# Kernel tuning notes

Measured on AMD Instinct MI355X. Metric: run time of the kernel, lower is better.

The kernel has to match this reference:

```python
import jax, jax.numpy as jnp
import numpy as np

N = 100000      # nodes
E = 1600000     # edges (avg degree 16)
EMB = 128
L = 3           # num_layers
NUM_OPS = 64
MAX_BW = 64     # max_bitwidth
P = 4           # max_num_params


def setup_inputs() -> dict:
    key = jax.random.key(0)
    ks = jax.random.split(key, 24)
    w = lambda k, s: jax.random.normal(k, s, jnp.float32) * 0.05
    return {
        "ops": jax.random.randint(ks[0], (N,), 0, NUM_OPS),
        "params": jax.random.randint(ks[1], (N, P), 0, MAX_BW),
        "edge_src": jax.random.randint(ks[2], (E,), 0, N),
        "edge_dst": jax.random.randint(ks[3], (E,), 0, N),
        "op_emb_table": w(ks[4], (NUM_OPS, EMB)),
        "param_emb_table": w(ks[5], (MAX_BW, EMB)),
        "opmlp_w1": w(ks[6], ((1 + P) * EMB, EMB)), "opmlp_b1": w(ks[7], (EMB,)),
        "opmlp_w2": w(ks[8], (EMB, EMB)), "opmlp_b2": w(ks[9], (EMB,)),
        "conv_w": w(ks[10], (L, EMB, EMB)), "conv_b": w(ks[11], (L, EMB)),
        "mlp_w1": w(ks[12], (L * EMB, EMB)), "mlp_b1": w(ks[13], (EMB,)),
        "mlp_w2": w(ks[14], (EMB, EMB)), "mlp_b2": w(ks[15], (EMB,)),
        "mlpinv_w1": w(ks[16], (L * EMB, EMB)), "mlpinv_b1": w(ks[17], (EMB,)),
        "mlpinv_w2": w(ks[18], (EMB, EMB)), "mlpinv_b2": w(ks[19], (EMB,)),
        "comb_w": w(ks[20], (2 * EMB, EMB)), "comb_b": w(ks[21], (EMB,)),
    }


def _lrelu(x):
    return jax.nn.leaky_relu(x)  # slope 0.01, matches nn.LeakyReLU default


def _gin_mean(feat, src, dst, w, b):
    # DGL GINConv(aggregator='mean', eps=0): apply_func(feat + mean_in_neighbors(feat))
    n = feat.shape[0]
    msg = jax.ops.segment_sum(feat[src], dst, num_segments=n)           # [N, EMB]
    deg = jax.ops.segment_sum(jnp.ones(src.shape, feat.dtype), dst, num_segments=n)
    agg = msg / jnp.maximum(deg, 1.0)[:, None]
    return _lrelu((feat + agg) @ w + b)


def reference(ops, params, edge_src, edge_dst,
              op_emb_table, param_emb_table,
              opmlp_w1, opmlp_b1, opmlp_w2, opmlp_b2,
              conv_w, conv_b,
              mlp_w1, mlp_b1, mlp_w2, mlp_b2,
              mlpinv_w1, mlpinv_b1, mlpinv_w2, mlpinv_b2,
              comb_w, comb_b):
    n = ops.shape[0]
    # OpEmb: cat([op_emb] + per-param embs) -> MLP
    op_e = op_emb_table[ops]                               # [N, EMB]
    par_e = param_emb_table[params].reshape(n, -1)         # [N, P*EMB]
    h = jnp.concatenate([op_e, par_e], axis=1)
    h = _lrelu(h @ opmlp_w1 + opmlp_b1) @ opmlp_w2 + opmlp_b2
    states = h
    states_inv = h  # op_emb called twice on same inputs in the original

    conv_outs = []
    for i in range(L):
        states = _gin_mean(states, edge_src, edge_dst, conv_w[i], conv_b[i])
        conv_outs.append(states.sum(axis=0))
    final_sum = states.sum(axis=0)

    conv_outs_inv = []
    for i in range(L):
        states_inv = _gin_mean(states_inv, edge_dst, edge_src, conv_w[i], conv_b[i])
        # NOTE: original code appends states.sum(dim=0) (the final forward states),
        # not states_inv -- faithfully reproduced.
        conv_outs_inv.append(final_sum)

    g_emb = _lrelu(jnp.concatenate(conv_outs) @ mlp_w1 + mlp_b1) @ mlp_w2 + mlp_b2
    g_inv_emb = _lrelu(jnp.concatenate(conv_outs_inv) @ mlpinv_w1 + mlpinv_b1) @ mlpinv_w2 + mlpinv_b2

    out1 = jnp.concatenate([g_emb, g_inv_emb]) @ comb_w + comb_b          # [EMB]
    out2 = jnp.concatenate([states, states_inv], axis=1) @ comb_w + comb_b  # [N, EMB]
    return (out1, out2)
```

## Files before the change

### kernel.cpp

```cpp
#include <hip/hip_runtime.h>


typedef unsigned int  uint;
typedef unsigned short ushort;
typedef float  f32x4  __attribute__((ext_vector_type(4)));
typedef short  bf16x8 __attribute__((ext_vector_type(8)));

#define ABITS 9
#define CAPB  12288
#define CHUNK 2048

__device__ __forceinline__ float lrelu(float x) { return x > 0.0f ? x : 0.01f * x; }
__device__ __forceinline__ ushort f2b(float x) {
    uint u = __float_as_uint(x);
    return (ushort)((u + 0x7fffu + ((u >> 16) & 1u)) >> 16);
}
__device__ __forceinline__ float lof(uint u) { return __uint_as_float(u << 16); }
__device__ __forceinline__ float hif(uint u) { return __uint_as_float(u & 0xffff0000u); }

__global__ void tables_kernel(const float* __restrict__ opT, const float* __restrict__ parT,
                              const float* __restrict__ W1, float* __restrict__ A)
{
    int b = blockIdx.x;
    int t = b >> 6, v = b & 63, j = threadIdx.x;
    const float* emb = (t == 0 ? opT : parT) + v * 128;
    const float* w = W1 + (size_t)t * 128 * 128;
    float acc = 0.f;
    for (int k = 0; k < 128; ++k) acc += emb[k] * w[k * 128 + j];
    A[(size_t)b * 128 + j] = acc;
}

__global__ void prep_w(const float* __restrict__ convw, const float* __restrict__ ow2,
                       const float* __restrict__ cw, ushort* __restrict__ Wt)
{
    int t = blockIdx.x * 256 + threadIdx.x;
    int img = t >> 14, idx = t & 16383;
    int k = idx >> 7, c = idx & 127;
    const float* src;
    if (img < 3)      src = convw + img * 16384;
    else if (img == 3) src = ow2;
    else              src = cw + (img - 4) * 16384;
    float v = src[k * 128 + c];
    int byteoff = (img << 15) + (c << 8) + ((((k >> 3) ^ (c & 7)) << 4)) + ((k & 7) << 1);
    Wt[byteoff >> 1] = f2b(v);
}

__global__ __launch_bounds__(256) void binpass_kernel(
    const int* __restrict__ esrc, const int* __restrict__ edst, int E, int nb,
    int* __restrict__ gcur, uint2* __restrict__ binbuf)
{
    __shared__ int hist[448];
    __shared__ int lstart[448];
    __shared__ int gbase[448];
    __shared__ int lcur[448];
    __shared__ int gsum[8];
    __shared__ uint sKey[CHUNK * 2];
    __shared__ uint sPay[CHUNK * 2];
    __shared__ ushort sBin[CHUNK * 2];
    int tid = threadIdx.x, lane = tid & 63;
    int nb2 = nb * 2;

    for (int chunk = blockIdx.x; (size_t)chunk * CHUNK < (size_t)E; chunk += gridDim.x) {
        int base = chunk * CHUNK;
        int cnt = min(CHUNK, E - base);
        for (int i = tid; i < 448; i += 256) hist[i] = 0;
        __syncthreads();
        int s[8], d[8];
        #pragma unroll
        for (int i = 0; i < 8; ++i) {
            int idx = i * 256 + tid;
            if (idx < cnt) {
                s[i] = esrc[base + idx];
                d[i] = edst[base + idx];
                atomicAdd(&hist[d[i] >> ABITS], 1);
                atomicAdd(&hist[nb + (s[i] >> ABITS)], 1);
            } else s[i] = -1;
        }
        __syncthreads();
        #pragma unroll
        for (int k = 0; k < 2; ++k) {
            int idx = k * 256 + tid;
            int v = (idx < 448) ? hist[idx] : 0;
            int p = v;
            #pragma unroll
            for (int sh = 1; sh < 64; sh <<= 1) { int t = __shfl_up(p, sh, 64); if (lane >= sh) p += t; }
            if (idx < 448) {
                lstart[idx] = p - v;
                if (lane == 63) gsum[idx >> 6] = p;
            }
        }
        __syncthreads();
        if (tid == 0) { int run = 0; for (int g = 0; g < 7; ++g) { int t = gsum[g]; gsum[g] = run; run += t; } }
        __syncthreads();
        #pragma unroll
        for (int k = 0; k < 2; ++k) {
            int idx = k * 256 + tid;
            if (idx < 448) lstart[idx] += gsum[idx >> 6];
        }
        __syncthreads();
        for (int i = tid; i < nb2; i += 256) {
            int h = hist[i];
            gbase[i] = h ? atomicAdd(&gcur[i], h) : 0;
            lcur[i] = lstart[i];
        }
        __syncthreads();
        #pragma unroll
        for (int i = 0; i < 8; ++i) {
            if (s[i] >= 0) {
                int bf = d[i] >> ABITS;
                int p = atomicAdd(&lcur[bf], 1);
                sKey[p] = (uint)d[i]; sPay[p] = (uint)s[i]; sBin[p] = (ushort)bf;
                int bi = nb + (s[i] >> ABITS);
                int q = atomicAdd(&lcur[bi], 1);
                sKey[q] = (uint)s[i]; sPay[q] = (uint)d[i]; sBin[q] = (ushort)bi;
            }
        }
        __syncthreads();
        int total = 2 * cnt;
        for (int p = tid; p < total; p += 256) {
            int b = sBin[p];
            int pos = gbase[b] + (p - lstart[b]);
            if (pos < CAPB) binbuf[(size_t)b * CAPB + pos] = make_uint2(sKey[p], sPay[p]);
        }
        __syncthreads();
    }
}

__global__ __launch_bounds__(256) void csrpass_kernel(
    const uint2* __restrict__ binbuf, const int* __restrict__ gcur, int nb, int N,
    int* __restrict__ csr_f, int* __restrict__ off_f, int* __restrict__ cnt_f,
    int* __restrict__ csr_i, int* __restrict__ off_i, int* __restrict__ cnt_i)
{
    __shared__ int hist[512];
    __shared__ int loff[512];
    __shared__ int cur[512];
    __shared__ int gsum[8];
    int b = blockIdx.x;
    int dir = (b >= nb) ? 1 : 0;
    int binLocal = dir ? b - nb : b;
    int node0 = binLocal << ABITS;
    int nn = min(512, N - node0);
    int tid = threadIdx.x, lane = tid & 63;
    int total = min(gcur[b], CAPB);
    const uint2* seg = binbuf + (size_t)b * CAPB;
    int* csr = dir ? csr_i : csr_f;
    int* off = dir ? off_i : off_f;
    int* cnt = dir ? cnt_i : cnt_f;

    for (int i = tid; i < 512; i += 256) hist[i] = 0;
    __syncthreads();
    for (int e = tid; e < total; e += 256) {
        uint2 kp = seg[e];
        atomicAdd(&hist[kp.x - (uint)node0], 1);
    }
    __syncthreads();
    #pragma unroll
    for (int k = 0; k < 2; ++k) {
        int idx = k * 256 + tid;
        int v = hist[idx];
        int p = v;
        #pragma unroll
        for (int sh = 1; sh < 64; sh <<= 1) { int t = __shfl_up(p, sh, 64); if (lane >= sh) p += t; }
        loff[idx] = p - v;
        if (lane == 63) gsum[idx >> 6] = p;
    }
    __syncthreads();
    if (tid == 0) { int run = 0; for (int g = 0; g < 8; ++g) { int t = gsum[g]; gsum[g] = run; run += t; } }
    __syncthreads();
    #pragma unroll
    for (int k = 0; k < 2; ++k) {
        int idx = k * 256 + tid;
        loff[idx] += gsum[idx >> 6];
    }
    __syncthreads();
    int csrBase = binLocal * CAPB;
    for (int i = tid; i < 512; i += 256) {
        cur[i] = loff[i];
        if (i < nn) { off[node0 + i] = csrBase + loff[i]; cnt[node0 + i] = hist[i]; }
    }
    __syncthreads();
    int* csrSeg = csr + csrBase;
    for (int e = tid; e < total; e += 256) {
        uint2 kp = seg[e];
        int p = atomicAdd(&cur[kp.x - (uint)node0], 1);
        csrSeg[p] = (int)kp.y;
    }
}

__global__ __launch_bounds__(256, 8) void agg2_kernel(
    const ushort* __restrict__ Sf, const ushort* __restrict__ Si,
    const int* __restrict__ csr_f, const int* __restrict__ off_f, const int* __restrict__ cnt_f,
    const int* __restrict__ csr_i, const int* __restrict__ off_i, const int* __restrict__ cnt_i,
    ushort* __restrict__ msgf, ushort* __restrict__ msgi, int N)
{
    int gw = (blockIdx.x * 256 + threadIdx.x) >> 6;
    int lane = threadIdx.x & 63;
    int dir = 0, g = gw;
    if (g >= N) { dir = 1; g -= N; if (g >= N) return; }
    const uint* Sp = (const uint*)(dir ? Si : Sf);
    const int* csr = dir ? csr_i : csr_f;
    int off = (dir ? off_i : off_f)[g];
    int deg = (dir ? cnt_i : cnt_f)[g];

    float ax = 0.f, ay = 0.f;
    int d = 0;
    for (; d + 8 <= deg; d += 8) {
        int n0 = csr[off + d + 0], n1 = csr[off + d + 1];
        int n2 = csr[off + d + 2], n3 = csr[off + d + 3];
        int n4 = csr[off + d + 4], n5 = csr[off + d + 5];
        int n6 = csr[off + d + 6], n7 = csr[off + d + 7];
        uint v0 = Sp[(size_t)n0 * 64 + lane];
        uint v1 = Sp[(size_t)n1 * 64 + lane];
        uint v2 = Sp[(size_t)n2 * 64 + lane];
        uint v3 = Sp[(size_t)n3 * 64 + lane];
        uint v4 = Sp[(size_t)n4 * 64 + lane];
        uint v5 = Sp[(size_t)n5 * 64 + lane];
        uint v6 = Sp[(size_t)n6 * 64 + lane];
        uint v7 = Sp[(size_t)n7 * 64 + lane];
        ax += ((lof(v0) + lof(v1)) + (lof(v2) + lof(v3)))
            + ((lof(v4) + lof(v5)) + (lof(v6) + lof(v7)));
        ay += ((hif(v0) + hif(v1)) + (hif(v2) + hif(v3)))
            + ((hif(v4) + hif(v5)) + (hif(v6) + hif(v7)));
    }
    if (d + 4 <= deg) {
        int n0 = csr[off + d + 0], n1 = csr[off + d + 1];
        int n2 = csr[off + d + 2], n3 = csr[off + d + 3];
        uint v0 = Sp[(size_t)n0 * 64 + lane];
        uint v1 = Sp[(size_t)n1 * 64 + lane];
        uint v2 = Sp[(size_t)n2 * 64 + lane];
        uint v3 = Sp[(size_t)n3 * 64 + lane];
        ax += (lof(v0) + lof(v1)) + (lof(v2) + lof(v3));
        ay += (hif(v0) + hif(v1)) + (hif(v2) + hif(v3));
        d += 4;
    }
    for (; d < deg; ++d) {
        uint v = Sp[(size_t)csr[off + d] * 64 + lane];
        ax += lof(v); ay += hif(v);
    }
    float invd = 1.0f / fmaxf((float)deg, 1.0f);
    uint self = Sp[(size_t)g * 64 + lane];
    ax = lof(self) + ax * invd;
    ay = hif(self) + ay * invd;
    uint pk = (uint)f2b(ax) | ((uint)f2b(ay) << 16);
    ((uint*)(dir ? msgi : msgf))[(size_t)g * 64 + lane] = pk;
}

__device__ __forceinline__ void stage_w(const ushort* __restrict__ img, ushort* ldsW, int tid)
{
    const uint4* s = (const uint4*)img;
    uint4* d = (uint4*)ldsW;
    #pragma unroll
    for (int i = 0; i < 4; ++i) d[tid + (i << 9)] = s[tid + (i << 9)];
}

__device__ __forceinline__ void mfma_gemm_128(const ushort* ldsA, const ushort* ldsW,
                                              int lane, int row0, f32x4 acc[8])
{
    int l15 = lane & 15, lg = lane >> 4;
    int arow = row0 + l15;
    const char* Ab = (const char*)ldsA + arow * 256;
    int akey = (arow & 7) << 4;
    #pragma unroll
    for (int kk = 0; kk < 4; ++kk) {
        bf16x8 af = *(const bf16x8*)(Ab + ((((kk << 2) + lg) << 4) ^ akey));
        #pragma unroll
        for (int ct = 0; ct < 8; ++ct) {
            int c = (ct << 4) + l15;
            const char* Bb = (const char*)ldsW + c * 256;
            bf16x8 bf = *(const bf16x8*)(Bb + ((((kk << 2) + lg) << 4) ^ ((c & 7) << 4)));
            acc[ct] = __builtin_amdgcn_mfma_f32_16x16x32_bf16(af, bf, acc[ct], 0, 0, 0);
        }
    }
}

__device__ __forceinline__ void stage_a_bf16(const ushort* __restrict__ S, ushort* ldsA,
                                             int node0, int tid, int N)
{
    #pragma unroll
    for (int i = 0; i < 4; ++i) {
        int chunk = tid + (i << 9);
        int r = chunk >> 4, cin = chunk & 15;
        int g = node0 + r;
        uint4 v;
        if (g < N) v = *(const uint4*)(S + (size_t)g * 128 + (cin << 3));
        else       { v.x = 0; v.y = 0; v.z = 0; v.w = 0; }
        *(uint4*)((char*)ldsA + r * 256 + ((cin ^ (r & 7)) << 4)) = v;
    }
}

__global__ __launch_bounds__(512, 4) void gemm2_kernel(
    const ushort* __restrict__ msgf, const ushort* __restrict__ msgi,
    ushort* __restrict__ Sf_out, ushort* __restrict__ Si_out,
    const ushort* __restrict__ Wimg, const float* __restrict__ bias,
    float* __restrict__ colsum, int N)
{
    __shared__ __align__(16) ushort ldsW[16384];
    __shared__ __align__(16) ushort ldsA[16384];
    __shared__ float ldsCS[128];
    int tid = threadIdx.x, lane = tid & 63, w = tid >> 6;
    bool fwd = (blockIdx.x & 1) == 0;
    int node0 = (blockIdx.x >> 1) << 7;
    const ushort* msg = fwd ? msgf : msgi;
    ushort* Sout = fwd ? Sf_out : Si_out;

    stage_w(Wimg, ldsW, tid);
    stage_a_bf16(msg, ldsA, node0, tid, N);
    if (fwd && tid < 128) ldsCS[tid] = 0.f;
    __syncthreads();

    f32x4 acc[8];
    #pragma unroll
    for (int i = 0; i < 8; ++i) acc[i] = f32x4{0.f, 0.f, 0.f, 0.f};
    mfma_gemm_128(ldsA, ldsW, lane, w << 4, acc);

    int l15 = lane & 15, lg = lane >> 4;
    #pragma unroll
    for (int ct = 0; ct < 8; ++ct) {
        int c = (ct << 4) + l15;
        float bb = bias[c];
        float csum = 0.f;
        #pragma unroll
        for (int j = 0; j < 4; ++j) {
            int g = node0 + (w << 4) + (lg << 2) + j;
            float o = lrelu(acc[ct][j] + bb);
            if (g < N) {
                Sout[(size_t)g * 128 + c] = f2b(o);
                csum += o;
            }
        }
        if (fwd) {
            csum += __shfl_xor(csum, 16);
            csum += __shfl_xor(csum, 32);
            if (lg == 0) atomicAdd(&ldsCS[c], csum);
        }
    }
    if (fwd) {
        __syncthreads();
        if (tid < 128) atomicAdd(&colsum[tid], ldsCS[tid]);
    }
}

__global__ __launch_bounds__(512, 4) void opemb_fused(
    const int* __restrict__ ops, const int* __restrict__ params,
    const float* __restrict__ Atab, const float* __restrict__ b1,
    const ushort* __restrict__ W2img, const float* __restrict__ b2,
    ushort* __restrict__ S0, ushort* __restrict__ S2, int N)
{
    __shared__ __align__(16) ushort ldsW[16384];
    __shared__ __align__(16) ushort ldsA[16384];
    int tid = threadIdx.x, lane = tid & 63, w = tid >> 6;
    int node0 = blockIdx.x << 7;

    stage_w(W2img, ldsW, tid);

    int r = tid >> 2, sub = tid & 3;
    int g = node0 + r;
    float4 acc4[8];
    if (g < N) {
        int op = ops[g];
        const float4* T = (const float4*)(Atab + ((size_t)op << 7) + (sub << 5));
        #pragma unroll
        for (int q = 0; q < 8; ++q) acc4[q] = T[q];
        #pragma unroll
        for (int p = 0; p < 4; ++p) {
            int pv = params[(g << 2) + p];
            const float4* Tp = (const float4*)(Atab + ((size_t)((p + 1) * 64 + pv) << 7) + (sub << 5));
            #pragma unroll
            for (int q = 0; q < 8; ++q) {
                float4 u = Tp[q];
                acc4[q].x += u.x; acc4[q].y += u.y; acc4[q].z += u.z; acc4[q].w += u.w;
            }
        }
        const float4* Bv = (const float4*)(b1 + (sub << 5));
        #pragma unroll
        for (int q = 0; q < 8; ++q) {
            float4 bb = Bv[q];
            acc4[q].x = lrelu(acc4[q].x + bb.x);
            acc4[q].y = lrelu(acc4[q].y + bb.y);
            acc4[q].z = lrelu(acc4[q].z + bb.z);
            acc4[q].w = lrelu(acc4[q].w + bb.w);
        }
    } else {
        #pragma unroll
        for (int q = 0; q < 8; ++q) acc4[q] = make_float4(0.f, 0.f, 0.f, 0.f);
    }
    int akey = r & 7;
    #pragma unroll
    for (int q2 = 0; q2 < 4; ++q2) {
        int ch = (sub << 2) + q2;
        float4 a = acc4[q2 * 2], b = acc4[q2 * 2 + 1];
        uint4 pk;
        pk.x = (uint)f2b(a.x) | ((uint)f2b(a.y) << 16);
        pk.y = (uint)f2b(a.z) | ((uint)f2b(a.w) << 16);
        pk.z = (uint)f2b(b.x) | ((uint)f2b(b.y) << 16);
        pk.w = (uint)f2b(b.z) | ((uint)f2b(b.w) << 16);
        *(uint4*)((char*)ldsA + r * 256 + ((ch ^ akey) << 4)) = pk;
    }
    __syncthreads();

    f32x4 acc[8];
    #pragma unroll
    for (int i = 0; i < 8; ++i) acc[i] = f32x4{0.f, 0.f, 0.f, 0.f};
    mfma_gemm_128(ldsA, ldsW, lane, w << 4, acc);

    int l15 = lane & 15, lg = lane >> 4;
    #pragma unroll
    for (int ct = 0; ct < 8; ++ct) {
        int c = (ct << 4) + l15;
        float bb = b2[c];
        #pragma unroll
        for (int j = 0; j < 4; ++j) {
            int gg = node0 + (w << 4) + (lg << 2) + j;
            if (gg < N) {
                ushort ob = f2b(acc[ct][j] + bb);
                S0[(size_t)gg * 128 + c] = ob;
                S2[(size_t)gg * 128 + c] = ob;
            }
        }
    }
}

__global__ __launch_bounds__(512, 4) void out2_fused(
    const ushort* __restrict__ Sf, const ushort* __restrict__ Si,
    const ushort* __restrict__ CWimg, const float* __restrict__ cb,
    float* __restrict__ out, int N)
{
    __shared__ __align__(16) ushort ldsW[16384];
    __shared__ __align__(16) ushort ldsA[16384];
    int tid = threadIdx.x, lane = tid & 63, w = tid >> 6;
    int node0 = blockIdx.x << 7;
    f32x4 acc[8];
    #pragma unroll
    for (int i = 0; i < 8; ++i) acc[i] = f32x4{0.f, 0.f, 0.f, 0.f};
    #pragma unroll
    for (int pass = 0; pass < 2; ++pass) {
        if (pass) __syncthreads();
        stage_w(CWimg + (pass << 14), ldsW, tid);
        stage_a_bf16(pass ? Si : Sf, ldsA, node0, tid, N);
        __syncthreads();
        mfma_gemm_128(ldsA, ldsW, lane, w << 4, acc);
    }
    int l15 = lane & 15, lg = lane >> 4;
    #pragma unroll
    for (int ct = 0; ct < 8; ++ct) {
        int c = (ct << 4) + l15;
        float bb = cb[c];
        #pragma unroll
        for (int j = 0; j < 4; ++j) {
            int g = node0 + (w << 4) + (lg << 2) + j;
            if (g < N) out[(size_t)g * 128 + c] = acc[ct][j] + bb;
        }
    }
}

__global__ void final_kernel(const float* __restrict__ convsum,
    const float* __restrict__ mw1, const float* __restrict__ mb1,
    const float* __restrict__ mw2, const float* __restrict__ mb2,
    const float* __restrict__ iw1, const float* __restrict__ ib1,
    const float* __restrict__ iw2, const float* __restrict__ ib2,
    const float* __restrict__ cw, const float* __restrict__ cb,
    float* __restrict__ out1)
{
    __shared__ float x[384];
    __shared__ float t1[128];
    __shared__ float t2[128];
    __shared__ float g1[128];
    __shared__ float g2[128];
    int j = threadIdx.x;
    x[j] = convsum[j]; x[128 + j] = convsum[128 + j]; x[256 + j] = convsum[256 + j];
    __syncthreads();
    float a = mb1[j];
    for (int k = 0; k < 384; ++k) a += x[k] * mw1[k * 128 + j];
    t1[j] = lrelu(a);
    float c = ib1[j];
    for (int k = 0; k < 384; ++k) c += x[256 + (k & 127)] * iw1[k * 128 + j];
    t2[j] = lrelu(c);
    __syncthreads();
    float b = mb2[j];
    float d = ib2[j];
    for (int k = 0; k < 128; ++k) {
        b += t1[k] * mw2[k * 128 + j];
        d += t2[k] * iw2[k * 128 + j];
    }
    g1[j] = b; g2[j] = d;
    __syncthreads();
    float e = cb[j];
    for (int k = 0; k < 128; ++k)
        e += g1[k] * cw[k * 128 + j] + g2[k] * cw[(128 + k) * 128 + j];
    out1[j] = e;
}

extern "C" void kernel_launch(void* const* d_in, const int* in_sizes, int n_in,
                              void* d_out, int out_size, void* d_ws, size_t ws_size,
                              hipStream_t stream)
{
    (void)n_in; (void)out_size; (void)ws_size;
    const int*   ops    = (const int*)d_in[0];
    const int*   params = (const int*)d_in[1];
    const int*   esrc   = (const int*)d_in[2];
    const int*   edst   = (const int*)d_in[3];
    const float* opT    = (const float*)d_in[4];
    const float* parT   = (const float*)d_in[5];
    const float* ow1    = (const float*)d_in[6];
    const float* ob1    = (const float*)d_in[7];
    const float* ow2    = (const float*)d_in[8];
    const float* ob2    = (const float*)d_in[9];
    const float* convw  = (const float*)d_in[10];
    const float* convb  = (const float*)d_in[11];
    const float* mw1    = (const float*)d_in[12];
    const float* mb1    = (const float*)d_in[13];
    const float* mw2    = (const float*)d_in[14];
    const float* mb2    = (const float*)d_in[15];
    const float* iw1    = (const float*)d_in[16];
    const float* ib1    = (const float*)d_in[17];
    const float* iw2    = (const float*)d_in[18];
    const float* ib2    = (const float*)d_in[19];
    const float* cw     = (const float*)d_in[20];
    const float* cb     = (const float*)d_in[21];

    const int N = in_sizes[0];
    const int E = in_sizes[2];
    const int nb = (N + 511) >> ABITS;
    const size_t NP = (size_t)N * 128;

    ushort* S0   = (ushort*)d_ws;
    ushort* S1   = S0 + NP;
    ushort* S2   = S1 + NP;
    ushort* S3   = S2 + NP;
    ushort* Wt   = S3 + NP;
    float*  Atab = (float*)(Wt + 6 * 16384);
    float*  convsum = Atab + 320 * 128;
    int*    gcur = (int*)(convsum + 512);
    uint2*  binbuf = (uint2*)(gcur + 512);
    int*    csr_f = (int*)(binbuf + (size_t)2 * nb * CAPB);
    int*    csr_i = csr_f + (size_t)nb * CAPB;
    int*    off_f = csr_i + (size_t)nb * CAPB;
    int*    cnt_f = off_f + N;
    int*    off_i = cnt_f + N;
    int*    cnt_i = off_i + N;

    float* out1 = (float*)d_out;
    float* out2 = out1 + 128;
    ushort* MSGF = (ushort*)out2;
    ushort* MSGI = MSGF + NP;

    hipMemsetAsync(convsum, 0, sizeof(float) * 1024, stream);

    tables_kernel<<<320, 128, 0, stream>>>(opT, parT, ow1, Atab);
    prep_w<<<384, 256, 0, stream>>>(convw, ow2, cw, Wt);
    binpass_kernel<<<(E + CHUNK - 1) / CHUNK, 256, 0, stream>>>(esrc, edst, E, nb, gcur, binbuf);
    csrpass_kernel<<<2 * nb, 256, 0, stream>>>(binbuf, gcur, nb, N,
                                               csr_f, off_f, cnt_f, csr_i, off_i, cnt_i);

    const int grid = (N + 127) / 128;
    opemb_fused<<<grid, 512, 0, stream>>>(ops, params, Atab, ob1, Wt + 3 * 16384, ob2, S0, S2, N);

    const int aggGrid = (2 * N + 3) / 4;
    agg2_kernel<<<aggGrid, 256, 0, stream>>>(S0, S2, csr_f, off_f, cnt_f, csr_i, off_i, cnt_i, MSGF, MSGI, N);
    gemm2_kernel<<<2 * grid, 512, 0, stream>>>(MSGF, MSGI, S1, S3, Wt,             convb,       convsum,       N);
    agg2_kernel<<<aggGrid, 256, 0, stream>>>(S1, S3, csr_f, off_f, cnt_f, csr_i, off_i, cnt_i, MSGF, MSGI, N);
    gemm2_kernel<<<2 * grid, 512, 0, stream>>>(MSGF, MSGI, S0, S2, Wt + 16384,     convb + 128, convsum + 128, N);
    agg2_kernel<<<aggGrid, 256, 0, stream>>>(S0, S2, csr_f, off_f, cnt_f, csr_i, off_i, cnt_i, MSGF, MSGI, N);
    gemm2_kernel<<<2 * grid, 512, 0, stream>>>(MSGF, MSGI, S1, S3, Wt + 2 * 16384, convb + 256, convsum + 256, N);

    final_kernel<<<1, 128, 0, stream>>>(convsum, mw1, mb1, mw2, mb2,
                                        iw1, ib1, iw2, ib2, cw, cb, out1);
    out2_fused<<<grid, 512, 0, stream>>>(S1, S3, Wt + 4 * 16384, cb, out2, N);
}
```

Measured before the change: 712.3 us.

## Two-level LDS radix sort in CSR pass to order neighbors by source bin

The CSR build kernel now does a first counting-sort pass in shared memory that orders each bin's edges by the high bits of the neighbor index. A second pass then scatters them into per-node CSR slots, so each node's neighbor list comes out roughly sorted by source bin. The aim is better cache locality for the later gather in the aggregation kernel. In exchange it uses about 72KB of LDS per block, which lowers occupancy, and adds a __syncthreads per 256-edge iteration.

```diff
diff --git a/kernel.cpp b/kernel.cpp
--- a/kernel.cpp
+++ b/kernel.cpp
@@ -131,33 +131,61 @@
     int* __restrict__ csr_f, int* __restrict__ off_f, int* __restrict__ cnt_f,
     int* __restrict__ csr_i, int* __restrict__ off_i, int* __restrict__ cnt_i)
 {
-    __shared__ int hist[512];
+    __shared__ ushort sKey[CAPB];
+    __shared__ uint   sPay[CAPB];
+    __shared__ int hist1[256];
+    __shared__ int cur1[256];
+    __shared__ int hist2[512];
     __shared__ int loff[512];
-    __shared__ int cur[512];
+    __shared__ int cur2[512];
     __shared__ int gsum[8];
     int b = blockIdx.x;
     int dir = (b >= nb) ? 1 : 0;
     int binLocal = dir ? b - nb : b;
     int node0 = binLocal << ABITS;
     int nn = min(512, N - node0);
-    int tid = threadIdx.x, lane = tid & 63;
+    int tid = threadIdx.x, lane = tid & 63, wv = tid >> 6;
     int total = min(gcur[b], CAPB);
     const uint2* seg = binbuf + (size_t)b * CAPB;
     int* csr = dir ? csr_i : csr_f;
     int* off = dir ? off_i : off_f;
     int* cnt = dir ? cnt_i : cnt_f;
 
-    for (int i = tid; i < 512; i += 256) hist[i] = 0;
+    hist1[tid] = 0;
+    hist2[tid] = 0; hist2[256 + tid] = 0;
     __syncthreads();
     for (int e = tid; e < total; e += 256) {
         uint2 kp = seg[e];
-        atomicAdd(&hist[kp.x - (uint)node0], 1);
-    }
-    __syncthreads();
+        atomicAdd(&hist1[kp.y >> ABITS], 1);
+        atomicAdd(&hist2[kp.x - (uint)node0], 1);
+    }
+    __syncthreads();
+    {
+        int v = hist1[tid];
+        int p = v;
+        #pragma unroll
+        for (int sh = 1; sh < 64; sh <<= 1) { int t = __shfl_up(p, sh, 64); if (lane >= sh) p += t; }
+        if (lane == 63) gsum[wv] = p;
+        __syncthreads();
+        if (tid == 0) { int run = 0; for (int g = 0; g < 4; ++g) { int t = gsum[g]; gsum[g] = run; run += t; } }
+        __syncthreads();
+        cur1[tid] = p - v + gsum[wv];
+    }
+    __syncthreads();
+    for (int base = 0; base < total; base += 256) {
+        int e = base + tid;
+        if (e < total) {
+            uint2 kp = seg[e];
+            int r1 = atomicAdd(&cur1[kp.y >> ABITS], 1);
+            sKey[r1] = (ushort)(kp.x - (uint)node0);
+            sPay[r1] = kp.y;
+        }
+        __syncthreads();
+    }
     #pragma unroll
     for (int k = 0; k < 2; ++k) {
         int idx = k * 256 + tid;
-        int v = hist[idx];
+        int v = hist2[idx];
         int p = v;
         #pragma unroll
         for (int sh = 1; sh < 64; sh <<= 1) { int t = __shfl_up(p, sh, 64); if (lane >= sh) p += t; }
@@ -175,15 +203,19 @@
     __syncthreads();
     int csrBase = binLocal * CAPB;
     for (int i = tid; i < 512; i += 256) {
-        cur[i] = loff[i];
-        if (i < nn) { off[node0 + i] = csrBase + loff[i]; cnt[node0 + i] = hist[i]; }
+        cur2[i] = loff[i];
+        if (i < nn) { off[node0 + i] = csrBase + loff[i]; cnt[node0 + i] = hist2[i]; }
     }
     __syncthreads();
     int* csrSeg = csr + csrBase;
-    for (int e = tid; e < total; e += 256) {
-        uint2 kp = seg[e];
-        int p = atomicAdd(&cur[kp.x - (uint)node0], 1);
-        csrSeg[p] = (int)kp.y;
+    for (int base = 0; base < total; base += 256) {
+        int p = base + tid;
+        if (p < total) {
+            int dl = sKey[p];
+            int r2 = atomicAdd(&cur2[dl], 1);
+            csrSeg[r2] = (int)sPay[p];
+        }
+        __syncthreads();
     }
 }
 
```

Result: slower. 733.0 us (+2.9%).

## Interleave forward and inverse GIN passes so GEMM and aggregation share launches

Applied to the files above, without the earlier changes.

Replaces the paired agg2/gemm2 launches with a staggered schedule. Each combined kernel runs the GEMM for one direction and the neighbour aggregation for the other direction in disjoint block ranges, so the compute-bound MFMA work and the memory-bound gather overlap within one launch. The aggregation now loads a batch of up to 64 CSR indices per wavefront and broadcasts them with readlane instead of doing a scalar load per neighbour. The GEMM reads its A operand straight from global memory instead of staging it in LDS, which cuts LDS use but may raise global traffic and the number of launches.

```diff
diff --git a/kernel.cpp b/kernel.cpp
--- a/kernel.cpp
+++ b/kernel.cpp
@@ -187,62 +187,65 @@
     }
 }
 
-__global__ __launch_bounds__(256, 8) void agg2_kernel(
-    const ushort* __restrict__ Sf, const ushort* __restrict__ Si,
-    const int* __restrict__ csr_f, const int* __restrict__ off_f, const int* __restrict__ cnt_f,
-    const int* __restrict__ csr_i, const int* __restrict__ off_i, const int* __restrict__ cnt_i,
-    ushort* __restrict__ msgf, ushort* __restrict__ msgi, int N)
-{
-    int gw = (blockIdx.x * 256 + threadIdx.x) >> 6;
-    int lane = threadIdx.x & 63;
-    int dir = 0, g = gw;
-    if (g >= N) { dir = 1; g -= N; if (g >= N) return; }
-    const uint* Sp = (const uint*)(dir ? Si : Sf);
-    const int* csr = dir ? csr_i : csr_f;
-    int off = (dir ? off_i : off_f)[g];
-    int deg = (dir ? cnt_i : cnt_f)[g];
-
+__device__ __forceinline__ void agg_body(
+    const ushort* __restrict__ Sin, const int* __restrict__ csr,
+    const int* __restrict__ offs, const int* __restrict__ cnt,
+    ushort* __restrict__ msg, int node, int lane, int N)
+{
+    if (node >= N) return;
+    const char* Sp = (const char*)Sin;
+    int off = __builtin_amdgcn_readfirstlane(offs[node]);
+    int deg = __builtin_amdgcn_readfirstlane(cnt[node]);
+    int lane4 = lane << 2;
     float ax = 0.f, ay = 0.f;
-    int d = 0;
-    for (; d + 8 <= deg; d += 8) {
-        int n0 = csr[off + d + 0], n1 = csr[off + d + 1];
-        int n2 = csr[off + d + 2], n3 = csr[off + d + 3];
-        int n4 = csr[off + d + 4], n5 = csr[off + d + 5];
-        int n6 = csr[off + d + 6], n7 = csr[off + d + 7];
-        uint v0 = Sp[(size_t)n0 * 64 + lane];
-        uint v1 = Sp[(size_t)n1 * 64 + lane];
-        uint v2 = Sp[(size_t)n2 * 64 + lane];
-        uint v3 = Sp[(size_t)n3 * 64 + lane];
-        uint v4 = Sp[(size_t)n4 * 64 + lane];
-        uint v5 = Sp[(size_t)n5 * 64 + lane];
-        uint v6 = Sp[(size_t)n6 * 64 + lane];
-        uint v7 = Sp[(size_t)n7 * 64 + lane];
-        ax += ((lof(v0) + lof(v1)) + (lof(v2) + lof(v3)))
-            + ((lof(v4) + lof(v5)) + (lof(v6) + lof(v7)));
-        ay += ((hif(v0) + hif(v1)) + (hif(v2) + hif(v3)))
-            + ((hif(v4) + hif(v5)) + (hif(v6) + hif(v7)));
-    }
-    if (d + 4 <= deg) {
-        int n0 = csr[off + d + 0], n1 = csr[off + d + 1];
-        int n2 = csr[off + d + 2], n3 = csr[off + d + 3];
-        uint v0 = Sp[(size_t)n0 * 64 + lane];
-        uint v1 = Sp[(size_t)n1 * 64 + lane];
-        uint v2 = Sp[(size_t)n2 * 64 + lane];
-        uint v3 = Sp[(size_t)n3 * 64 + lane];
-        ax += (lof(v0) + lof(v1)) + (lof(v2) + lof(v3));
-        ay += (hif(v0) + hif(v1)) + (hif(v2) + hif(v3));
-        d += 4;
-    }
-    for (; d < deg; ++d) {
-        uint v = Sp[(size_t)csr[off + d] * 64 + lane];
-        ax += lof(v); ay += hif(v);
+    for (int base = 0; base < deg; base += 64) {
+        int rem = deg - base;
+        int cl = min(lane, rem - 1);
+        int idxv = csr[off + base + cl];
+        int bcnt = min(rem, 64);
+        int j = 0;
+        for (; j + 8 <= bcnt; j += 8) {
+            int n0 = __builtin_amdgcn_readlane(idxv, j + 0);
+            int n1 = __builtin_amdgcn_readlane(idxv, j + 1);
+            int n2 = __builtin_amdgcn_readlane(idxv, j + 2);
+            int n3 = __builtin_amdgcn_readlane(idxv, j + 3);
+            int n4 = __builtin_amdgcn_readlane(idxv, j + 4);
+            int n5 = __builtin_amdgcn_readlane(idxv, j + 5);
+            int n6 = __builtin_amdgcn_readlane(idxv, j + 6);
+            int n7 = __builtin_amdgcn_readlane(idxv, j + 7);
+            uint v0 = *(const uint*)(Sp + ((size_t)(uint)n0 << 8) + lane4);
+            uint v1 = *(const uint*)(Sp + ((size_t)(uint)n1 << 8) + lane4);
+            uint v2 = *(const uint*)(Sp + ((size_t)(uint)n2 << 8) + lane4);
+            uint v3 = *(const uint*)(Sp + ((size_t)(uint)n3 << 8) + lane4);
+            uint v4 = *(const uint*)(Sp + ((size_t)(uint)n4 << 8) + lane4);
+            uint v5 = *(const uint*)(Sp + ((size_t)(uint)n5 << 8) + lane4);
+            uint v6 = *(const uint*)(Sp + ((size_t)(uint)n6 << 8) + lane4);
+            uint v7 = *(const uint*)(Sp + ((size_t)(uint)n7 << 8) + lane4);
+            ax += ((lof(v0) + lof(v1)) + (lof(v2) + lof(v3)))
+                + ((lof(v4) + lof(v5)) + (lof(v6) + lof(v7)));
+            ay += ((hif(v0) + hif(v1)) + (hif(v2) + hif(v3)))
+                + ((hif(v4) + hif(v5)) + (hif(v6) + hif(v7)));
+        }
+        for (; j < bcnt; ++j) {
+            int n = __builtin_amdgcn_readlane(idxv, j);
+            uint v = *(const uint*)(Sp + ((size_t)(uint)n << 8) + lane4);
+            ax += lof(v); ay += hif(v);
+        }
     }
     float invd = 1.0f / fmaxf((float)deg, 1.0f);
-    uint self = Sp[(size_t)g * 64 + lane];
+    uint self = *(const uint*)(Sp + ((size_t)(uint)node << 8) + lane4);
     ax = lof(self) + ax * invd;
     ay = hif(self) + ay * invd;
-    uint pk = (uint)f2b(ax) | ((uint)f2b(ay) << 16);
-    ((uint*)(dir ? msgi : msgf))[(size_t)g * 64 + lane] = pk;
+    ((uint*)msg)[(size_t)node * 64 + lane] = (uint)f2b(ax) | ((uint)f2b(ay) << 16);
+}
+
+__global__ __launch_bounds__(256, 8) void agg1_kernel(
+    const ushort* __restrict__ Sin, const int* __restrict__ csr,
+    const int* __restrict__ offs, const int* __restrict__ cnt,
+    ushort* __restrict__ msg, int N)
+{
+    int node = (blockIdx.x << 2) + (threadIdx.x >> 6);
+    agg_body(Sin, csr, offs, cnt, msg, node, threadIdx.x & 63, N);
 }
 
 __device__ __forceinline__ void stage_w(const ushort* __restrict__ img, ushort* ldsW, int tid)
@@ -253,16 +256,26 @@
     for (int i = 0; i < 4; ++i) d[tid + (i << 9)] = s[tid + (i << 9)];
 }
 
-__device__ __forceinline__ void mfma_gemm_128(const ushort* ldsA, const ushort* ldsW,
-                                              int lane, int row0, f32x4 acc[8])
-{
+template <bool COLSUM>
+__device__ __forceinline__ void gemm_body(
+    const ushort* __restrict__ msg, ushort* __restrict__ Sout,
+    const ushort* __restrict__ Wimg, const float* __restrict__ bias,
+    float* __restrict__ colsum, int node0, int tid,
+    ushort* ldsW, float* ldsCS, int N)
+{
+    int lane = tid & 63, w = tid >> 6;
+    stage_w(Wimg, ldsW, tid);
+    if (COLSUM && tid < 128) ldsCS[tid] = 0.f;
+    __syncthreads();
     int l15 = lane & 15, lg = lane >> 4;
-    int arow = row0 + l15;
-    const char* Ab = (const char*)ldsA + arow * 256;
-    int akey = (arow & 7) << 4;
+    int gr = min(node0 + (w << 4) + l15, N - 1);
+    const char* Ab = (const char*)msg + ((size_t)gr << 8);
+    f32x4 acc[8];
+    #pragma unroll
+    for (int i = 0; i < 8; ++i) acc[i] = f32x4{0.f, 0.f, 0.f, 0.f};
     #pragma unroll
     for (int kk = 0; kk < 4; ++kk) {
-        bf16x8 af = *(const bf16x8*)(Ab + ((((kk << 2) + lg) << 4) ^ akey));
+        bf16x8 af = *(const bf16x8*)(Ab + (((kk << 2) + lg) << 4));
         #pragma unroll
         for (int ct = 0; ct < 8; ++ct) {
             int c = (ct << 4) + l15;
@@ -271,49 +284,6 @@
             acc[ct] = __builtin_amdgcn_mfma_f32_16x16x32_bf16(af, bf, acc[ct], 0, 0, 0);
         }
     }
-}
-
-__device__ __forceinline__ void stage_a_bf16(const ushort* __restrict__ S, ushort* ldsA,
-                                             int node0, int tid, int N)
-{
-    #pragma unroll
-    for (int i = 0; i < 4; ++i) {
-        int chunk = tid + (i << 9);
-        int r = chunk >> 4, cin = chunk & 15;
-        int g = node0 + r;
-        uint4 v;
-        if (g < N) v = *(const uint4*)(S + (size_t)g * 128 + (cin << 3));
-        else       { v.x = 0; v.y = 0; v.z = 0; v.w = 0; }
-        *(uint4*)((char*)ldsA + r * 256 + ((cin ^ (r & 7)) << 4)) = v;
-    }
-}
-
-__global__ __launch_bounds__(512, 4) void gemm2_kernel(
-    const ushort* __restrict__ msgf, const ushort* __restrict__ msgi,
-    ushort* __restrict__ Sf_out, ushort* __restrict__ Si_out,
-    const ushort* __restrict__ Wimg, const float* __restrict__ bias,
-    float* __restrict__ colsum, int N)
-{
-    __shared__ __align__(16) ushort ldsW[16384];
-    __shared__ __align__(16) ushort ldsA[16384];
-    __shared__ float ldsCS[128];
-    int tid = threadIdx.x, lane = tid & 63, w = tid >> 6;
-    bool fwd = (blockIdx.x & 1) == 0;
-    int node0 = (blockIdx.x >> 1) << 7;
-    const ushort* msg = fwd ? msgf : msgi;
-    ushort* Sout = fwd ? Sf_out : Si_out;
-
-    stage_w(Wimg, ldsW, tid);
-    stage_a_bf16(msg, ldsA, node0, tid, N);
-    if (fwd && tid < 128) ldsCS[tid] = 0.f;
-    __syncthreads();
-
-    f32x4 acc[8];
-    #pragma unroll
-    for (int i = 0; i < 8; ++i) acc[i] = f32x4{0.f, 0.f, 0.f, 0.f};
-    mfma_gemm_128(ldsA, ldsW, lane, w << 4, acc);
-
-    int l15 = lane & 15, lg = lane >> 4;
     #pragma unroll
     for (int ct = 0; ct < 8; ++ct) {
         int c = (ct << 4) + l15;
@@ -328,15 +298,36 @@
                 csum += o;
             }
         }
-        if (fwd) {
+        if (COLSUM) {
             csum += __shfl_xor(csum, 16);
             csum += __shfl_xor(csum, 32);
             if (lg == 0) atomicAdd(&ldsCS[c], csum);
         }
     }
-    if (fwd) {
+    if (COLSUM) {
         __syncthreads();
         if (tid < 128) atomicAdd(&colsum[tid], ldsCS[tid]);
+    }
+}
+
+template <bool COLSUM>
+__global__ __launch_bounds__(512, 4) void comb_kernel(
+    const ushort* __restrict__ msg_g, ushort* __restrict__ Sout,
+    const ushort* __restrict__ Wimg, const float* __restrict__ bias,
+    float* __restrict__ colsum,
+    const ushort* __restrict__ Sin_a, const int* __restrict__ csr,
+    const int* __restrict__ offs, const int* __restrict__ cnt,
+    ushort* __restrict__ msg_a, int gemmBlocks, int N)
+{
+    __shared__ __align__(16) ushort ldsW[16384];
+    __shared__ float ldsCS[128];
+    int tid = threadIdx.x;
+    if ((int)blockIdx.x < gemmBlocks) {
+        gemm_body<COLSUM>(msg_g, Sout, Wimg, bias, colsum,
+                          (int)blockIdx.x << 7, tid, ldsW, ldsCS, N);
+    } else {
+        int node = (((int)blockIdx.x - gemmBlocks) << 3) + (tid >> 6);
+        agg_body(Sin_a, csr, offs, cnt, msg_a, node, tid & 63, N);
     }
 }
 
@@ -344,7 +335,7 @@
     const int* __restrict__ ops, const int* __restrict__ params,
     const float* __restrict__ Atab, const float* __restrict__ b1,
     const ushort* __restrict__ W2img, const float* __restrict__ b2,
-    ushort* __restrict__ S0, ushort* __restrict__ S2, int N)
+    ushort* __restrict__ S0, int N)
 {
     __shared__ __align__(16) ushort ldsW[16384];
     __shared__ __align__(16) ushort ldsA[16384];
@@ -398,12 +389,24 @@
     }
     __syncthreads();
 
+    int l15 = lane & 15, lg = lane >> 4;
+    int arow = (w << 4) + l15;
+    const char* Ab = (const char*)ldsA + arow * 256;
+    int akey2 = (arow & 7) << 4;
     f32x4 acc[8];
     #pragma unroll
     for (int i = 0; i < 8; ++i) acc[i] = f32x4{0.f, 0.f, 0.f, 0.f};
-    mfma_gemm_128(ldsA, ldsW, lane, w << 4, acc);
-
-    int l15 = lane & 15, lg = lane >> 4;
+    #pragma unroll
+    for (int kk = 0; kk < 4; ++kk) {
+        bf16x8 af = *(const bf16x8*)(Ab + ((((kk << 2) + lg) << 4) ^ akey2));
+        #pragma unroll
+        for (int ct = 0; ct < 8; ++ct) {
+            int c = (ct << 4) + l15;
+            const char* Bb = (const char*)ldsW + c * 256;
+            bf16x8 bf = *(const bf16x8*)(Bb + ((((kk << 2) + lg) << 4) ^ ((c & 7) << 4)));
+            acc[ct] = __builtin_amdgcn_mfma_f32_16x16x32_bf16(af, bf, acc[ct], 0, 0, 0);
+        }
+    }
     #pragma unroll
     for (int ct = 0; ct < 8; ++ct) {
         int c = (ct << 4) + l15;
@@ -411,12 +414,23 @@
         #pragma unroll
         for (int j = 0; j < 4; ++j) {
             int gg = node0 + (w << 4) + (lg << 2) + j;
-            if (gg < N) {
-                ushort ob = f2b(acc[ct][j] + bb);
-                S0[(size_t)gg * 128 + c] = ob;
-                S2[(size_t)gg * 128 + c] = ob;
-            }
-        }
+            if (gg < N) S0[(size_t)gg * 128 + c] = f2b(acc[ct][j] + bb);
+        }
+    }
+}
+
+__device__ __forceinline__ void stage_a_bf16(const ushort* __restrict__ S, ushort* ldsA,
+                                             int node0, int tid, int N)
+{
+    #pragma unroll
+    for (int i = 0; i < 4; ++i) {
+        int chunk = tid + (i << 9);
+        int r = chunk >> 4, cin = chunk & 15;
+        int g = node0 + r;
+        uint4 v;
+        if (g < N) v = *(const uint4*)(S + (size_t)g * 128 + (cin << 3));
+        else       { v.x = 0; v.y = 0; v.z = 0; v.w = 0; }
+        *(uint4*)((char*)ldsA + r * 256 + ((cin ^ (r & 7)) << 4)) = v;
     }
 }
 
@@ -432,15 +446,28 @@
     f32x4 acc[8];
     #pragma unroll
     for (int i = 0; i < 8; ++i) acc[i] = f32x4{0.f, 0.f, 0.f, 0.f};
+    int l15 = lane & 15, lg = lane >> 4;
     #pragma unroll
     for (int pass = 0; pass < 2; ++pass) {
         if (pass) __syncthreads();
         stage_w(CWimg + (pass << 14), ldsW, tid);
         stage_a_bf16(pass ? Si : Sf, ldsA, node0, tid, N);
         __syncthreads();
-        mfma_gemm_128(ldsA, ldsW, lane, w << 4, acc);
-    }
-    int l15 = lane & 15, lg = lane >> 4;
+        int arow = (w << 4) + l15;
+        const char* Ab = (const char*)ldsA + arow * 256;
+        int akey = (arow & 7) << 4;
+        #pragma unroll
+        for (int kk = 0; kk < 4; ++kk) {
+            bf16x8 af = *(const bf16x8*)(Ab + ((((kk << 2) + lg) << 4) ^ akey));
+            #pragma unroll
+            for (int ct = 0; ct < 8; ++ct) {
+                int c = (ct << 4) + l15;
+                const char* Bb = (const char*)ldsW + c * 256;
+                bf16x8 bf = *(const bf16x8*)(Bb + ((((kk << 2) + lg) << 4) ^ ((c & 7) << 4)));
+                acc[ct] = __builtin_amdgcn_mfma_f32_16x16x32_bf16(af, bf, acc[ct], 0, 0, 0);
+            }
+        }
+    }
     #pragma unroll
     for (int ct = 0; ct < 8; ++ct) {
         int c = (ct << 4) + l15;
@@ -552,18 +579,31 @@
     csrpass_kernel<<<2 * nb, 256, 0, stream>>>(binbuf, gcur, nb, N,
                                                csr_f, off_f, cnt_f, csr_i, off_i, cnt_i);
 
-    const int grid = (N + 127) / 128;
-    opemb_fused<<<grid, 512, 0, stream>>>(ops, params, Atab, ob1, Wt + 3 * 16384, ob2, S0, S2, N);
-
-    const int aggGrid = (2 * N + 3) / 4;
-    agg2_kernel<<<aggGrid, 256, 0, stream>>>(S0, S2, csr_f, off_f, cnt_f, csr_i, off_i, cnt_i, MSGF, MSGI, N);
-    gemm2_kernel<<<2 * grid, 512, 0, stream>>>(MSGF, MSGI, S1, S3, Wt,             convb,       convsum,       N);
-    agg2_kernel<<<aggGrid, 256, 0, stream>>>(S1, S3, csr_f, off_f, cnt_f, csr_i, off_i, cnt_i, MSGF, MSGI, N);
-    gemm2_kernel<<<2 * grid, 512, 0, stream>>>(MSGF, MSGI, S0, S2, Wt + 16384,     convb + 128, convsum + 128, N);
-    agg2_kernel<<<aggGrid, 256, 0, stream>>>(S0, S2, csr_f, off_f, cnt_f, csr_i, off_i, cnt_i, MSGF, MSGI, N);
-    gemm2_kernel<<<2 * grid, 512, 0, stream>>>(MSGF, MSGI, S1, S3, Wt + 2 * 16384, convb + 256, convsum + 256, N);
+    const int gemmBlocks = (N + 127) / 128;
+    const int aggBlocks  = (N + 7) / 8;
+    const int combGrid   = gemmBlocks + aggBlocks;
+
+    opemb_fused<<<gemmBlocks, 512, 0, stream>>>(ops, params, Atab, ob1, Wt + 3 * 16384, ob2, S0, N);
+
+    const ushort* W0 = Wt;
+    const ushort* W1i = Wt + 16384;
+    const ushort* W2i = Wt + 2 * 16384;
+
+    agg1_kernel<<<(N + 3) / 4, 256, 0, stream>>>(S0, csr_f, off_f, cnt_f, MSGF, N);
+    comb_kernel<true ><<<combGrid, 512, 0, stream>>>(MSGF, S1, W0, convb, convsum,
+                                                     S0, csr_i, off_i, cnt_i, MSGI, gemmBlocks, N);
+    comb_kernel<false><<<combGrid, 512, 0, stream>>>(MSGI, S3, W0, convb, nullptr,
+                                                     S1, csr_f, off_f, cnt_f, MSGF, gemmBlocks, N);
+    comb_kernel<true ><<<combGrid, 512, 0, stream>>>(MSGF, S0, W1i, convb + 128, convsum + 128,
+                                                     S3, csr_i, off_i, cnt_i, MSGI, gemmBlocks, N);
+    comb_kernel<false><<<combGrid, 512, 0, stream>>>(MSGI, S2, W1i, convb + 128, nullptr,
+                                                     S0, csr_f, off_f, cnt_f, MSGF, gemmBlocks, N);
+    comb_kernel<true ><<<combGrid, 512, 0, stream>>>(MSGF, S1, W2i, convb + 256, convsum + 256,
+                                                     S2, csr_i, off_i, cnt_i, MSGI, gemmBlocks, N);
+    comb_kernel<false><<<gemmBlocks, 512, 0, stream>>>(MSGI, S3, W2i, convb + 256, nullptr,
+                                                       S2, csr_i, off_i, cnt_i, MSGI, gemmBlocks, N);
 
     final_kernel<<<1, 128, 0, stream>>>(convsum, mw1, mb1, mw2, mb2,
                                         iw1, ib1, iw2, ib2, cw, cb, out1);
-    out2_fused<<<grid, 512, 0, stream>>>(S1, S3, Wt + 4 * 16384, cb, out2, N);
-}
+    out2_fused<<<gemmBlocks, 512, 0, stream>>>(S1, S3, Wt + 4 * 16384, cb, out2, N);
+}
```

New measurement: 712.6 us. About the same (+0.0%).

## Swap MFMA operands to load activations directly from global and drop S2 copy

Applied to the files above, without the earlier changes.

The dense GEMM kernels now treat the weight tile in LDS as the A operand and read each node's activation row straight from global memory as the B operand. This removes the activation LDS staging buffer and one barrier, and raises the occupancy hint to 8. The transposed accumulator layout lets each lane write 4 contiguous channels as packed bf16 or float4 stores, with column sums reduced through 16-lane shuffles. The opemb kernel no longer writes a duplicate S2 copy, since the first aggregation reads S0 for both directions. The trade-off is uncached per-lane global loads inside the MFMA loop in place of coalesced staging.

```diff
diff --git a/kernel.cpp b/kernel.cpp
--- a/kernel.cpp
+++ b/kernel.cpp
@@ -253,49 +253,13 @@
     for (int i = 0; i < 4; ++i) d[tid + (i << 9)] = s[tid + (i << 9)];
 }
 
-__device__ __forceinline__ void mfma_gemm_128(const ushort* ldsA, const ushort* ldsW,
-                                              int lane, int row0, f32x4 acc[8])
-{
-    int l15 = lane & 15, lg = lane >> 4;
-    int arow = row0 + l15;
-    const char* Ab = (const char*)ldsA + arow * 256;
-    int akey = (arow & 7) << 4;
-    #pragma unroll
-    for (int kk = 0; kk < 4; ++kk) {
-        bf16x8 af = *(const bf16x8*)(Ab + ((((kk << 2) + lg) << 4) ^ akey));
-        #pragma unroll
-        for (int ct = 0; ct < 8; ++ct) {
-            int c = (ct << 4) + l15;
-            const char* Bb = (const char*)ldsW + c * 256;
-            bf16x8 bf = *(const bf16x8*)(Bb + ((((kk << 2) + lg) << 4) ^ ((c & 7) << 4)));
-            acc[ct] = __builtin_amdgcn_mfma_f32_16x16x32_bf16(af, bf, acc[ct], 0, 0, 0);
-        }
-    }
-}
-
-__device__ __forceinline__ void stage_a_bf16(const ushort* __restrict__ S, ushort* ldsA,
-                                             int node0, int tid, int N)
-{
-    #pragma unroll
-    for (int i = 0; i < 4; ++i) {
-        int chunk = tid + (i << 9);
-        int r = chunk >> 4, cin = chunk & 15;
-        int g = node0 + r;
-        uint4 v;
-        if (g < N) v = *(const uint4*)(S + (size_t)g * 128 + (cin << 3));
-        else       { v.x = 0; v.y = 0; v.z = 0; v.w = 0; }
-        *(uint4*)((char*)ldsA + r * 256 + ((cin ^ (r & 7)) << 4)) = v;
-    }
-}
-
-__global__ __launch_bounds__(512, 4) void gemm2_kernel(
+__global__ __launch_bounds__(512, 8) void gemm2_kernel(
     const ushort* __restrict__ msgf, const ushort* __restrict__ msgi,
     ushort* __restrict__ Sf_out, ushort* __restrict__ Si_out,
     const ushort* __restrict__ Wimg, const float* __restrict__ bias,
     float* __restrict__ colsum, int N)
 {
     __shared__ __align__(16) ushort ldsW[16384];
-    __shared__ __align__(16) ushort ldsA[16384];
     __shared__ float ldsCS[128];
     int tid = threadIdx.x, lane = tid & 63, w = tid >> 6;
     bool fwd = (blockIdx.x & 1) == 0;
@@ -304,34 +268,60 @@
     ushort* Sout = fwd ? Sf_out : Si_out;
 
     stage_w(Wimg, ldsW, tid);
-    stage_a_bf16(msg, ldsA, node0, tid, N);
     if (fwd && tid < 128) ldsCS[tid] = 0.f;
     __syncthreads();
 
+    int l15 = lane & 15, lg = lane >> 4;
+    int node = node0 + (w << 4) + l15;
+    int gr = min(node, N - 1);
+    const char* Bb = (const char*)msg + ((size_t)gr << 8);
+
     f32x4 acc[8];
     #pragma unroll
     for (int i = 0; i < 8; ++i) acc[i] = f32x4{0.f, 0.f, 0.f, 0.f};
-    mfma_gemm_128(ldsA, ldsW, lane, w << 4, acc);
-
-    int l15 = lane & 15, lg = lane >> 4;
+    #pragma unroll
+    for (int kk = 0; kk < 4; ++kk) {
+        bf16x8 bfr = *(const bf16x8*)(Bb + (((kk << 2) + lg) << 4));
+        #pragma unroll
+        for (int ct = 0; ct < 8; ++ct) {
+            int c = (ct << 4) + l15;
+            const char* Ab = (const char*)ldsW + c * 256;
+            bf16x8 af = *(const bf16x8*)(Ab + ((((kk << 2) + lg) << 4) ^ ((c & 7) << 4)));
+            acc[ct] = __builtin_amdgcn_mfma_f32_16x16x32_bf16(af, bfr, acc[ct], 0, 0, 0);
+        }
+    }
+
+    bool valid = node < N;
     #pragma unroll
     for (int ct = 0; ct < 8; ++ct) {
-        int c = (ct << 4) + l15;
-        float bb = bias[c];
-        float csum = 0.f;
-        #pragma unroll
-        for (int j = 0; j < 4; ++j) {
-            int g = node0 + (w << 4) + (lg << 2) + j;
-            float o = lrelu(acc[ct][j] + bb);
-            if (g < N) {
-                Sout[(size_t)g * 128 + c] = f2b(o);
-                csum += o;
+        int ch0 = (ct << 4) + (lg << 2);
+        float4 bb = *(const float4*)(bias + ch0);
+        float o0 = lrelu(acc[ct][0] + bb.x);
+        float o1 = lrelu(acc[ct][1] + bb.y);
+        float o2 = lrelu(acc[ct][2] + bb.z);
+        float o3 = lrelu(acc[ct][3] + bb.w);
+        if (valid) {
+            uint2 pk;
+            pk.x = (uint)f2b(o0) | ((uint)f2b(o1) << 16);
+            pk.y = (uint)f2b(o2) | ((uint)f2b(o3) << 16);
+            *(uint2*)((char*)Sout + ((size_t)node << 8) + (ch0 << 1)) = pk;
+        }
+        if (fwd) {
+            float c0 = valid ? o0 : 0.f, c1 = valid ? o1 : 0.f;
+            float c2 = valid ? o2 : 0.f, c3 = valid ? o3 : 0.f;
+            #pragma unroll
+            for (int m = 1; m < 16; m <<= 1) {
+                c0 += __shfl_xor(c0, m);
+                c1 += __shfl_xor(c1, m);
+                c2 += __shfl_xor(c2, m);
+                c3 += __shfl_xor(c3, m);
             }
-        }
-        if (fwd) {
-            csum += __shfl_xor(csum, 16);
-            csum += __shfl_xor(csum, 32);
-            if (lg == 0) atomicAdd(&ldsCS[c], csum);
+            if (l15 == 0) {
+                atomicAdd(&ldsCS[ch0 + 0], c0);
+                atomicAdd(&ldsCS[ch0 + 1], c1);
+                atomicAdd(&ldsCS[ch0 + 2], c2);
+                atomicAdd(&ldsCS[ch0 + 3], c3);
+            }
         }
     }
     if (fwd) {
@@ -344,7 +334,7 @@
     const int* __restrict__ ops, const int* __restrict__ params,
     const float* __restrict__ Atab, const float* __restrict__ b1,
     const ushort* __restrict__ W2img, const float* __restrict__ b2,
-    ushort* __restrict__ S0, ushort* __restrict__ S2, int N)
+    ushort* __restrict__ S0, int N)
 {
     __shared__ __align__(16) ushort ldsW[16384];
     __shared__ __align__(16) ushort ldsA[16384];
@@ -398,37 +388,49 @@
     }
     __syncthreads();
 
+    int l15 = lane & 15, lg = lane >> 4;
+    int node = node0 + (w << 4) + l15;
+    int brow = (w << 4) + l15;
+    const char* Bb = (const char*)ldsA + brow * 256;
+    int bkey = (brow & 7) << 4;
     f32x4 acc[8];
     #pragma unroll
     for (int i = 0; i < 8; ++i) acc[i] = f32x4{0.f, 0.f, 0.f, 0.f};
-    mfma_gemm_128(ldsA, ldsW, lane, w << 4, acc);
-
-    int l15 = lane & 15, lg = lane >> 4;
-    #pragma unroll
-    for (int ct = 0; ct < 8; ++ct) {
-        int c = (ct << 4) + l15;
-        float bb = b2[c];
-        #pragma unroll
-        for (int j = 0; j < 4; ++j) {
-            int gg = node0 + (w << 4) + (lg << 2) + j;
-            if (gg < N) {
-                ushort ob = f2b(acc[ct][j] + bb);
-                S0[(size_t)gg * 128 + c] = ob;
-                S2[(size_t)gg * 128 + c] = ob;
-            }
-        }
-    }
-}
-
-__global__ __launch_bounds__(512, 4) void out2_fused(
+    #pragma unroll
+    for (int kk = 0; kk < 4; ++kk) {
+        bf16x8 bfr = *(const bf16x8*)(Bb + ((((kk << 2) + lg) << 4) ^ bkey));
+        #pragma unroll
+        for (int ct = 0; ct < 8; ++ct) {
+            int c = (ct << 4) + l15;
+            const char* Ab = (const char*)ldsW + c * 256;
+            bf16x8 af = *(const bf16x8*)(Ab + ((((kk << 2) + lg) << 4) ^ ((c & 7) << 4)));
+            acc[ct] = __builtin_amdgcn_mfma_f32_16x16x32_bf16(af, bfr, acc[ct], 0, 0, 0);
+        }
+    }
+    if (node < N) {
+        #pragma unroll
+        for (int ct = 0; ct < 8; ++ct) {
+            int ch0 = (ct << 4) + (lg << 2);
+            float4 bb = *(const float4*)(b2 + ch0);
+            uint2 pk;
+            pk.x = (uint)f2b(acc[ct][0] + bb.x) | ((uint)f2b(acc[ct][1] + bb.y) << 16);
+            pk.y = (uint)f2b(acc[ct][2] + bb.z) | ((uint)f2b(acc[ct][3] + bb.w) << 16);
+            *(uint2*)((char*)S0 + ((size_t)node << 8) + (ch0 << 1)) = pk;
+        }
+    }
+}
+
+__global__ __launch_bounds__(512, 8) void out2_fused(
     const ushort* __restrict__ Sf, const ushort* __restrict__ Si,
     const ushort* __restrict__ CWimg, const float* __restrict__ cb,
     float* __restrict__ out, int N)
 {
     __shared__ __align__(16) ushort ldsW[16384];
-    __shared__ __align__(16) ushort ldsA[16384];
     int tid = threadIdx.x, lane = tid & 63, w = tid >> 6;
     int node0 = blockIdx.x << 7;
+    int l15 = lane & 15, lg = lane >> 4;
+    int node = node0 + (w << 4) + l15;
+    int gr = min(node, N - 1);
     f32x4 acc[8];
     #pragma unroll
     for (int i = 0; i < 8; ++i) acc[i] = f32x4{0.f, 0.f, 0.f, 0.f};
@@ -436,19 +438,31 @@
     for (int pass = 0; pass < 2; ++pass) {
         if (pass) __syncthreads();
         stage_w(CWimg + (pass << 14), ldsW, tid);
-        stage_a_bf16(pass ? Si : Sf, ldsA, node0, tid, N);
-        __syncthreads();
-        mfma_gemm_128(ldsA, ldsW, lane, w << 4, acc);
-    }
-    int l15 = lane & 15, lg = lane >> 4;
-    #pragma unroll
-    for (int ct = 0; ct < 8; ++ct) {
-        int c = (ct << 4) + l15;
-        float bb = cb[c];
-        #pragma unroll
-        for (int j = 0; j < 4; ++j) {
-            int g = node0 + (w << 4) + (lg << 2) + j;
-            if (g < N) out[(size_t)g * 128 + c] = acc[ct][j] + bb;
+        __syncthreads();
+        const char* Bb = (const char*)(pass ? Si : Sf) + ((size_t)gr << 8);
+        #pragma unroll
+        for (int kk = 0; kk < 4; ++kk) {
+            bf16x8 bfr = *(const bf16x8*)(Bb + (((kk << 2) + lg) << 4));
+            #pragma unroll
+            for (int ct = 0; ct < 8; ++ct) {
+                int c = (ct << 4) + l15;
+                const char* Ab = (const char*)ldsW + c * 256;
+                bf16x8 af = *(const bf16x8*)(Ab + ((((kk << 2) + lg) << 4) ^ ((c & 7) << 4)));
+                acc[ct] = __builtin_amdgcn_mfma_f32_16x16x32_bf16(af, bfr, acc[ct], 0, 0, 0);
+            }
+        }
+    }
+    if (node < N) {
+        #pragma unroll
+        for (int ct = 0; ct < 8; ++ct) {
+            int ch0 = (ct << 4) + (lg << 2);
+            float4 bb = *(const float4*)(cb + ch0);
+            float4 o;
+            o.x = acc[ct][0] + bb.x;
+            o.y = acc[ct][1] + bb.y;
+            o.z = acc[ct][2] + bb.z;
+            o.w = acc[ct][3] + bb.w;
+            *(float4*)(out + (size_t)node * 128 + ch0) = o;
         }
     }
 }
@@ -553,10 +567,10 @@
                                                csr_f, off_f, cnt_f, csr_i, off_i, cnt_i);
 
     const int grid = (N + 127) / 128;
-    opemb_fused<<<grid, 512, 0, stream>>>(ops, params, Atab, ob1, Wt + 3 * 16384, ob2, S0, S2, N);
+    opemb_fused<<<grid, 512, 0, stream>>>(ops, params, Atab, ob1, Wt + 3 * 16384, ob2, S0, N);
 
     const int aggGrid = (2 * N + 3) / 4;
-    agg2_kernel<<<aggGrid, 256, 0, stream>>>(S0, S2, csr_f, off_f, cnt_f, csr_i, off_i, cnt_i, MSGF, MSGI, N);
+    agg2_kernel<<<aggGrid, 256, 0, stream>>>(S0, S0, csr_f, off_f, cnt_f, csr_i, off_i, cnt_i, MSGF, MSGI, N);
     gemm2_kernel<<<2 * grid, 512, 0, stream>>>(MSGF, MSGI, S1, S3, Wt,             convb,       convsum,       N);
     agg2_kernel<<<aggGrid, 256, 0, stream>>>(S1, S3, csr_f, off_f, cnt_f, csr_i, off_i, cnt_i, MSGF, MSGI, N);
     gemm2_kernel<<<2 * grid, 512, 0, stream>>>(MSGF, MSGI, S0, S2, Wt + 16384,     convb + 128, convsum + 128, N);
```

Result: faster. 687.4 us (-3.5%).
